# Performance work log

Hardware: AMD Instinct MI355X
Metric: run time of the kernel (lower is better)

Reference implementation:

```python
import jax, jax.numpy as jnp
import numpy as np

N_STEPS = 100
TAU_S = 5.0  # network_config['tau_s']
SHAPE = (16, 128, 16, 16, N_STEPS)  # [B, C, H, W, T]


def psp(target):
    """Leaky-integrator postsynaptic potential: syn_t = syn_{t-1}*(1-1/tau_s) + x_t, emit syn_t/tau_s."""
    x = jnp.moveaxis(target, -1, 0)  # time-major [T, B, C, H, W]
    decay = 1.0 - 1.0 / TAU_S

    def step(syn, xt):
        syn = syn * decay + xt
        return syn, syn / TAU_S

    _, syns = jax.lax.scan(step, jnp.zeros_like(x[0]), x)
    return jnp.moveaxis(syns, 0, -1)  # back to [B, C, H, W, T]


def setup_inputs() -> dict:
    key = jax.random.key(0)
    k1, k2 = jax.random.split(key)
    outputs = jax.random.normal(k1, SHAPE, dtype=jnp.float32) * 0.1
    target = (jax.random.uniform(k2, SHAPE) < 0.2).astype(jnp.float32)
    return {"outputs": outputs, "target": target}


def reference(outputs, target):
    # SpikeLoss.spike_kernel: 0.5 * sum((outputs - psp(target))**2)
    delta = outputs - psp(target)
    return 0.5 * jnp.sum(delta ** 2)
```

## Files before the change

kernel.cpp:

```cpp
#include <hip/hip_runtime.h>


#define T_STEPS 100
#define SEG 25
#define NPB 64
#define BLOCK 256
#define N_NEURONS (16 * 128 * 16 * 16)
#define GRID_P (N_NEURONS / NPB)
#define F4_PER_CHUNK (NPB * T_STEPS / 4)

__device__ __forceinline__ float block_loss(const float* __restrict__ outputs,
                                            const float* __restrict__ target) {
  __shared__ float lbuf[NPB * T_STEPS];
  __shared__ float lE[NPB * 4];
  __shared__ float wsum[BLOCK / 64];

  const int tid = threadIdx.x;
  const size_t base = (size_t)blockIdx.x * (NPB * T_STEPS);
  const float4* gt = reinterpret_cast<const float4*>(target + base);
  const float4* go = reinterpret_cast<const float4*>(outputs + base);
  float4* lb4 = reinterpret_cast<float4*>(lbuf);

  float4 bt[6];
#pragma unroll
  for (int k = 0; k < 6; ++k) bt[k] = gt[tid + 256 * k];
  float4 tt = make_float4(0.f, 0.f, 0.f, 0.f);
  if (tid < F4_PER_CHUNK - 1536) tt = gt[1536 + tid];
#pragma unroll
  for (int k = 0; k < 6; ++k) lb4[tid + 256 * k] = bt[k];
  if (tid < F4_PER_CHUNK - 1536) lb4[1536 + tid] = tt;

  float4 bo[6];
#pragma unroll
  for (int k = 0; k < 6; ++k) bo[k] = go[tid + 256 * k];
  float4 to = make_float4(0.f, 0.f, 0.f, 0.f);
  if (tid < F4_PER_CHUNK - 1536) to = go[1536 + tid];

  __syncthreads();

  const int n = tid >> 2;
  const int s = tid & 3;
  const float* xrow = lbuf + n * T_STEPS + s * SEG;
  float x[SEG];
#pragma unroll
  for (int j = 0; j < SEG; ++j) x[j] = xrow[j];
  float E = 0.f;
#pragma unroll
  for (int j = 0; j < SEG; ++j) E = fmaf(E, 0.8f, x[j]);
  lE[tid] = E;

  __syncthreads();

#pragma unroll
  for (int k = 0; k < 6; ++k) lb4[tid + 256 * k] = bo[k];
  if (tid < F4_PER_CHUNK - 1536) lb4[1536 + tid] = to;

  const float A25 = 3.77789319e-3f;
  const float A50 = 1.42724769e-5f;
  float carry = 0.f;
  if (s >= 1) carry = lE[tid - 1];
  if (s >= 2) carry = fmaf(A25, lE[tid - 2], carry);
  if (s >= 3) carry = fmaf(A50, lE[tid - 3], carry);

  __syncthreads();

  const float* orow = lbuf + n * T_STEPS + s * SEG;
  float syn = carry;
  float acc = 0.f;
#pragma unroll
  for (int j = 0; j < SEG; ++j) {
    syn = fmaf(syn, 0.8f, x[j]);
    float d = fmaf(-0.2f, syn, orow[j]);
    acc = fmaf(d, d, acc);
  }

#pragma unroll
  for (int off = 32; off > 0; off >>= 1) acc += __shfl_down(acc, off, 64);
  const int lane = tid & 63;
  const int wid = tid >> 6;
  if (lane == 0) wsum[wid] = acc;
  __syncthreads();
  return wsum[0] + wsum[1] + wsum[2] + wsum[3];
}

__global__ __launch_bounds__(BLOCK, 4) void spike_loss_partial(
    const float* __restrict__ outputs,
    const float* __restrict__ target,
    float* __restrict__ partial) {
  float blocksum = block_loss(outputs, target);
  if (threadIdx.x == 0) partial[blockIdx.x] = blocksum;
}

__global__ __launch_bounds__(256) void spike_loss_final(
    const float* __restrict__ partial, float* __restrict__ out, int nparts) {
  float acc = 0.0f;
  for (int i = threadIdx.x; i < nparts; i += 256) acc += partial[i];
#pragma unroll
  for (int off = 32; off > 0; off >>= 1) acc += __shfl_down(acc, off, 64);
  __shared__ float wsum[4];
  const int lane = threadIdx.x & 63;
  const int wid = threadIdx.x >> 6;
  if (lane == 0) wsum[wid] = acc;
  __syncthreads();
  if (threadIdx.x == 0) out[0] = 0.5f * (wsum[0] + wsum[1] + wsum[2] + wsum[3]);
}

__global__ __launch_bounds__(BLOCK, 4) void spike_loss_atomic(
    const float* __restrict__ outputs,
    const float* __restrict__ target,
    float* __restrict__ out) {
  float blocksum = block_loss(outputs, target);
  if (threadIdx.x == 0) atomicAdd(out, 0.5f * blocksum);
}

extern "C" void kernel_launch(void* const* d_in, const int* in_sizes, int n_in,
                              void* d_out, int out_size, void* d_ws, size_t ws_size,
                              hipStream_t stream) {
  const float* outputs = (const float*)d_in[0];
  const float* target = (const float*)d_in[1];
  float* out = (float*)d_out;

  if (ws_size >= GRID_P * sizeof(float)) {
    float* partial = (float*)d_ws;
    spike_loss_partial<<<GRID_P, BLOCK, 0, stream>>>(outputs, target, partial);
    spike_loss_final<<<1, 256, 0, stream>>>(partial, out, GRID_P);
  } else {
    hipMemsetAsync(out, 0, sizeof(float), stream);
    spike_loss_atomic<<<GRID_P, BLOCK, 0, stream>>>(outputs, target, out);
  }
}
```

Before: 433.4 us.

## Load both inputs directly into LDS with async global_load_lds

Replaces register-staged global loads with __builtin_amdgcn_global_load_lds, which copies both target and outputs straight into two separate LDS buffers. This removes the register round-trip and one barrier, and lets both arrays stream in at once. LDS use per block doubles to about 51KB, and launch bounds drop to 3 blocks per CU, which may cut occupancy for this memory-bound kernel. The x values are now re-read from LDS in the second pass instead of being held in registers.

```diff
diff --git a/kernel.cpp b/kernel.cpp
--- a/kernel.cpp
+++ b/kernel.cpp
@@ -7,11 +7,20 @@
 #define BLOCK 256
 #define N_NEURONS (16 * 128 * 16 * 16)
 #define GRID_P (N_NEURONS / NPB)
-#define F4_PER_CHUNK (NPB * T_STEPS / 4)
+#define F4_PER_ARR (NPB * T_STEPS / 4)
+
+#define GLOBAL_AS __attribute__((address_space(1)))
+#define LDS_AS __attribute__((address_space(3)))
+
+__device__ __forceinline__ void async_f4(const float4* g, float4* l) {
+  __builtin_amdgcn_global_load_lds((const GLOBAL_AS void*)g, (LDS_AS void*)l,
+                                   16, 0, 0);
+}
 
 __device__ __forceinline__ float block_loss(const float* __restrict__ outputs,
                                             const float* __restrict__ target) {
-  __shared__ float lbuf[NPB * T_STEPS];
+  __shared__ float xbuf[NPB * T_STEPS];
+  __shared__ float obuf[NPB * T_STEPS];
   __shared__ float lE[NPB * 4];
   __shared__ float wsum[BLOCK / 64];
 
@@ -19,41 +28,27 @@
   const size_t base = (size_t)blockIdx.x * (NPB * T_STEPS);
   const float4* gt = reinterpret_cast<const float4*>(target + base);
   const float4* go = reinterpret_cast<const float4*>(outputs + base);
-  float4* lb4 = reinterpret_cast<float4*>(lbuf);
+  float4* lx4 = reinterpret_cast<float4*>(xbuf);
+  float4* lo4 = reinterpret_cast<float4*>(obuf);
 
-  float4 bt[6];
 #pragma unroll
-  for (int k = 0; k < 6; ++k) bt[k] = gt[tid + 256 * k];
-  float4 tt = make_float4(0.f, 0.f, 0.f, 0.f);
-  if (tid < F4_PER_CHUNK - 1536) tt = gt[1536 + tid];
+  for (int it = 0; it < 6; ++it) async_f4(gt + it * 256 + tid, lx4 + it * 256 + tid);
+  if (tid < F4_PER_ARR - 1536) async_f4(gt + 1536 + tid, lx4 + 1536 + tid);
 #pragma unroll
-  for (int k = 0; k < 6; ++k) lb4[tid + 256 * k] = bt[k];
-  if (tid < F4_PER_CHUNK - 1536) lb4[1536 + tid] = tt;
-
-  float4 bo[6];
-#pragma unroll
-  for (int k = 0; k < 6; ++k) bo[k] = go[tid + 256 * k];
-  float4 to = make_float4(0.f, 0.f, 0.f, 0.f);
-  if (tid < F4_PER_CHUNK - 1536) to = go[1536 + tid];
+  for (int it = 0; it < 6; ++it) async_f4(go + it * 256 + tid, lo4 + it * 256 + tid);
+  if (tid < F4_PER_ARR - 1536) async_f4(go + 1536 + tid, lo4 + 1536 + tid);
 
   __syncthreads();
 
   const int n = tid >> 2;
   const int s = tid & 3;
-  const float* xrow = lbuf + n * T_STEPS + s * SEG;
-  float x[SEG];
-#pragma unroll
-  for (int j = 0; j < SEG; ++j) x[j] = xrow[j];
+  const float* xrow = xbuf + n * T_STEPS + s * SEG;
   float E = 0.f;
 #pragma unroll
-  for (int j = 0; j < SEG; ++j) E = fmaf(E, 0.8f, x[j]);
+  for (int j = 0; j < SEG; ++j) E = fmaf(E, 0.8f, xrow[j]);
   lE[tid] = E;
 
   __syncthreads();
-
-#pragma unroll
-  for (int k = 0; k < 6; ++k) lb4[tid + 256 * k] = bo[k];
-  if (tid < F4_PER_CHUNK - 1536) lb4[1536 + tid] = to;
 
   const float A25 = 3.77789319e-3f;
   const float A50 = 1.42724769e-5f;
@@ -62,14 +57,12 @@
   if (s >= 2) carry = fmaf(A25, lE[tid - 2], carry);
   if (s >= 3) carry = fmaf(A50, lE[tid - 3], carry);
 
-  __syncthreads();
-
-  const float* orow = lbuf + n * T_STEPS + s * SEG;
+  const float* orow = obuf + n * T_STEPS + s * SEG;
   float syn = carry;
   float acc = 0.f;
 #pragma unroll
   for (int j = 0; j < SEG; ++j) {
-    syn = fmaf(syn, 0.8f, x[j]);
+    syn = fmaf(syn, 0.8f, xrow[j]);
     float d = fmaf(-0.2f, syn, orow[j]);
     acc = fmaf(d, d, acc);
   }
@@ -83,7 +76,7 @@
   return wsum[0] + wsum[1] + wsum[2] + wsum[3];
 }
 
-__global__ __launch_bounds__(BLOCK, 4) void spike_loss_partial(
+__global__ __launch_bounds__(BLOCK, 3) void spike_loss_partial(
     const float* __restrict__ outputs,
     const float* __restrict__ target,
     float* __restrict__ partial) {
@@ -105,7 +98,7 @@
   if (threadIdx.x == 0) out[0] = 0.5f * (wsum[0] + wsum[1] + wsum[2] + wsum[3]);
 }
 
-__global__ __launch_bounds__(BLOCK, 4) void spike_loss_atomic(
+__global__ __launch_bounds__(BLOCK, 3) void spike_loss_atomic(
     const float* __restrict__ outputs,
     const float* __restrict__ target,
     float* __restrict__ out) {
```

Result: faster. 409.2 us (-5.6%).
